# Performance work log

Hardware: AMD Instinct MI355X
Metric: run time of the kernel (lower is better)

## Reference

```python
import jax, jax.numpy as jnp
import numpy as np

MARGIN = 1.0
SAFE_RADIUS = 4.0
B, C, H, W = 16, 48, 64, 64
N_CORR = 2048


def _normalize(x, eps=1e-12):
    # F.normalize(x, dim=0): L2-normalize over the channel axis
    return x / jnp.maximum(jnp.linalg.norm(x, axis=0, keepdims=True), eps)


def _grid_positions(h, w):
    i, j = jnp.meshgrid(jnp.arange(h, dtype=jnp.float32),
                        jnp.arange(w, dtype=jnp.float32), indexing='ij')
    return jnp.stack([i.reshape(-1), j.reshape(-1)], axis=0)


def _per_image(df1, df2, att1, att2, ids, fp2):
    c, h1, w1 = df1.shape
    _, h2, w2 = df2.shape
    all_d1 = _normalize(df1.reshape(c, -1))   # [c, h1*w1]
    all_d2 = _normalize(df2.reshape(c, -1))   # [c, h2*w2]

    d1 = all_d1[:, ids]                       # [c, n] gathered anchors
    s1 = att1.reshape(-1)[ids]                # [n]
    d2 = _normalize(df2[:, fp2[0], fp2[1]])   # [c, n] gathered positives

    positive_distance = 2.0 - 2.0 * jnp.sum(d1 * d2, axis=0)  # [n]

    # hard-negative mining in image 2
    grid2 = _grid_positions(h2, w2)           # [2, h2*w2]
    pd2 = jnp.max(jnp.abs(fp2.astype(jnp.float32)[:, :, None] - grid2[:, None, :]), axis=0)
    out2 = (pd2 > SAFE_RADIUS).astype(df1.dtype)            # [n, h2*w2]
    dm2 = 2.0 - 2.0 * jnp.einsum('cn,cm->nm', d1, all_d2)   # [n, h2*w2]
    neg2 = jnp.min(dm2 + (1.0 - out2) * 10.0, axis=1)       # [n]

    # hard-negative mining in image 1
    grid1 = _grid_positions(h1, w1)
    fp1 = grid1[:, ids]                                      # [2, n]
    pd1 = jnp.max(jnp.abs(fp1[:, :, None] - grid1[:, None, :]), axis=0)
    out1 = (pd1 > SAFE_RADIUS).astype(df1.dtype)
    dm1 = 2.0 - 2.0 * jnp.einsum('cn,cm->nm', d2, all_d1)
    neg1 = jnp.min(dm1 + (1.0 - out1) * 10.0, axis=1)

    diff = positive_distance - jnp.minimum(neg1, neg2)
    s2 = att2[0, fp2[0], fp2[1]]
    w = s1 * s2
    return jnp.sum(w * jax.nn.relu(MARGIN + diff)) / jnp.sum(w)


def setup_inputs() -> dict:
    key = jax.random.key(0)
    k1, k2, k3, k4, k5, k6 = jax.random.split(key, 6)
    return {
        'x1_encoded': jax.random.normal(k1, (B, C, H, W), dtype=jnp.float32),
        'x2_encoded': jax.random.normal(k2, (B, C, H, W), dtype=jnp.float32),
        'attentions1': jax.random.uniform(k3, (B, 1, H, W), dtype=jnp.float32),
        'attentions2': jax.random.uniform(k4, (B, 1, H, W), dtype=jnp.float32),
        'ids': jax.random.randint(k5, (B, N_CORR), 0, H * W),
        'fmap_pos2': jax.random.randint(k6, (B, 2, N_CORR), 0, H),
    }


def reference(x1_encoded, x2_encoded, attentions1, attentions2, ids, fmap_pos2):
    per_image = jax.vmap(_per_image)(x1_encoded, x2_encoded, attentions1,
                                     attentions2, ids, fmap_pos2)
    return jnp.mean(per_image).reshape(1)
```

## Files before the change

### kernel.cpp

```cpp
#include <hip/hip_runtime.h>
#include <stdint.h>

#define BB 16
#define HW 4096
#define NC 2048
#define KB 96
#define GRPB 12288
#define IMGB 393216

typedef __attribute__((ext_vector_type(8))) __bf16 bf16x8;
typedef __attribute__((ext_vector_type(8))) short short8;
typedef __attribute__((ext_vector_type(4))) float floatx4;

static __device__ __forceinline__ unsigned short f2bf(float f) {
    unsigned u = __builtin_bit_cast(unsigned, f);
    unsigned r = u + 0x7fffu + ((u >> 16) & 1u);
    return (unsigned short)(r >> 16);
}

#define GLD16(g, l) __builtin_amdgcn_global_load_lds((const __attribute__((address_space(1))) void*)(g), (__attribute__((address_space(3))) void*)(l), 16, 0, 0)

__global__ void prep_fused(const float* __restrict__ x1, const float* __restrict__ x2,
                           const int* __restrict__ ids, const int* __restrict__ fp2,
                           unsigned short* __restrict__ dbp,
                           int* __restrict__ perm, int* __restrict__ qcol_s,
                           int* __restrict__ aqpack, unsigned int* __restrict__ maxs2enc,
                           unsigned int* __restrict__ done) {
    __shared__ __align__(16) unsigned char slab[24576 + 4096 + 1024];
    int bid = blockIdx.x, tid = threadIdx.x;
    if (bid < 512) {
        int img = bid >> 8;
        int b = (bid >> 4) & 15;
        int p0 = (bid & 15) * 256;
        int w = tid >> 6, l = tid & 63;
        const float* x = img ? x2 : x1;
        const float* base = x + ((size_t)b * 48 + w * 12) * HW + p0 + 4 * l;
        floatx4 v[12];
        floatx4 ps = {0.f, 0.f, 0.f, 0.f};
#pragma unroll
        for (int cc = 0; cc < 12; ++cc) {
            v[cc] = *(const floatx4*)(base + cc * HW);
#pragma unroll
            for (int q = 0; q < 4; ++q) ps[q] = fmaf(v[cc][q], v[cc][q], ps[q]);
        }
        float* psum = (float*)(slab + 24576);
        float* rbuf = (float*)(slab + 24576 + 4096);
        *(floatx4*)(psum + w * 256 + 4 * l) = ps;
        __syncthreads();
        float s = psum[tid] + psum[256 + tid] + psum[512 + tid] + psum[768 + tid];
        rbuf[tid] = 1.f / fmaxf(sqrtf(s), 1e-12f);
        __syncthreads();
        floatx4 rv = *(const floatx4*)(rbuf + 4 * l);
#pragma unroll
        for (int q = 0; q < 4; ++q) {
            unsigned u[6];
#pragma unroll
            for (int p = 0; p < 6; ++p) {
                u[p] = (unsigned)f2bf(v[2 * p][q] * rv[q]) |
                       ((unsigned)f2bf(v[2 * p + 1][q] * rv[q]) << 16);
            }
            unsigned char* dst = slab + (4 * l + q) * KB + w * 24;
            *(uint2*)(dst + 0)  = make_uint2(u[0], u[1]);
            *(uint2*)(dst + 8)  = make_uint2(u[2], u[3]);
            *(uint2*)(dst + 16) = make_uint2(u[4], u[5]);
        }
        __syncthreads();
        unsigned char* dstb = (unsigned char*)dbp + (size_t)(img * BB + b) * IMGB
                              + (p0 >> 7) * GRPB;
#pragma unroll
        for (int i = 0; i < 6; ++i) {
            int L = i * 4096 + tid * 16;
            int g = L / GRPB;
            int r = L - g * GRPB;
            int k = r >> 11;
            int c = (r & 2047) >> 4;
            *(floatx4*)(dstb + L) = *(const floatx4*)(slab + (g * 128 + c) * KB + k * 16);
        }
    } else if (bid < 544) {
        int* hist = (int*)slab;
        int* base = hist + 64;
        int seg = bid - 512;
        int dir = seg >> 4, b = seg & 15;
        if (tid < 64) hist[tid] = 0;
        __syncthreads();
#pragma unroll
        for (int k = 0; k < 8; ++k) {
            int n = k * 256 + tid;
            int idv = ids[b * NC + n];
            int i2 = fp2[b * 2 * NC + n];
            int qi = (dir == 0) ? i2 : (idv >> 6);
            atomicAdd(&hist[qi], 1);
        }
        __syncthreads();
        if (tid == 0) {
            int run = 0;
            for (int k = 0; k < 64; ++k) { base[k] = run; run += hist[k]; }
        }
        __syncthreads();
#pragma unroll
        for (int k = 0; k < 8; ++k) {
            int n = k * 256 + tid;
            int idv = ids[b * NC + n];
            int i2 = fp2[b * 2 * NC + n];
            int j2 = fp2[b * 2 * NC + NC + n];
            int qi, qj, qcol;
            if (dir == 0) { qi = i2; qj = j2; qcol = idv; }
            else          { qi = idv >> 6; qj = idv & 63; qcol = i2 * 64 + j2; }
            int slot = atomicAdd(&base[qi], 1);
            perm[seg * NC + slot] = n;
            qcol_s[seg * NC + slot] = qcol;
            aqpack[seg * NC + slot] = (qi << 8) | qj;
        }
    } else {
        int t = (bid - 544) * 256 + tid;
        uint4* p = (uint4*)maxs2enc;
        uint4 z = {0u, 0u, 0u, 0u};
#pragma unroll
        for (int k = 0; k < 8; ++k) p[k * 2048 + t] = z;
        if (t == 0) done[0] = 0u;
    }
}

#define TILEB 12288

static __device__ __forceinline__ void dma_tile(const unsigned char* g, unsigned char* l,
                                                int wave, int lane) {
#pragma unroll
    for (int rr = 0; rr < 3; ++rr)
        GLD16(g + rr * 4096 + wave * 1024 + lane * 16, l + rr * 4096 + wave * 1024);
}

__global__ __launch_bounds__(256, 4) void maxscore_mfma(
    const unsigned short* __restrict__ dbp,
    const int* __restrict__ perm, const int* __restrict__ qcol_s,
    const int* __restrict__ aqpack, unsigned int* __restrict__ maxs2enc) {
    __shared__ __align__(16) unsigned char smem[2 * TILEB];

    int tid = threadIdx.x, wave = tid >> 6, lane = tid & 63;
    int quad = lane >> 4, cl = lane & 15;
    int gid = blockIdx.x;
    int seg = gid & 31, dir = seg >> 4, b = seg & 15;
    int rest = gid >> 5, mtile = rest & 7, nq = rest >> 3;
    int qbase = mtile * 256;
    int dbimg = 1 - dir;

    const unsigned char* dbQ = (const unsigned char*)dbp + (size_t)(dir * BB + b) * IMGB;
    short8 z8 = {0, 0, 0, 0, 0, 0, 0, 0};
    short8 afr[4][2];
#pragma unroll
    for (int t = 0; t < 4; ++t) {
        int slot = qbase + wave * 64 + t * 16 + cl;
        int qc = qcol_s[seg * NC + slot];
        const unsigned char* src = dbQ + (qc >> 7) * GRPB + (qc & 127) * 16;
        afr[t][0] = *(const short8*)(src + quad * 2048);
        afr[t][1] = z8;
        if (quad < 2) afr[t][1] = *(const short8*)(src + (4 + quad) * 2048);
    }
    float qif[4][4], qjc[4][4];
    float cl_f = (float)cl;
#pragma unroll
    for (int t = 0; t < 4; ++t)
#pragma unroll
        for (int r = 0; r < 4; ++r) {
            int slot = qbase + wave * 64 + t * 16 + quad * 4 + r;
            int ap = aqpack[seg * NC + slot];
            qif[t][r] = (float)(ap >> 8);
            qjc[t][r] = (float)(ap & 255) - cl_f;
        }
    int wb = seg * NC + qbase + wave * 64;
    int qimin = __builtin_amdgcn_readfirstlane(aqpack[wb] >> 8);
    int qimax = __builtin_amdgcn_readfirstlane(aqpack[wb + 63] >> 8);

    const unsigned char* dbase = (const unsigned char*)dbp + (size_t)(dbimg * BB + b) * IMGB;
    dma_tile(dbase + (size_t)nq * GRPB, smem, wave, lane);

    const floatx4 zf = {0.f, 0.f, 0.f, 0.f};
    float mx[4][4];
#pragma unroll
    for (int t = 0; t < 4; ++t)
#pragma unroll
        for (int r = 0; r < 4; ++r) mx[t][r] = -1e30f;

    int b0_off = quad * 2048 + cl * 16;
    int b1_off = (4 + (quad & 1)) * 2048 + cl * 16;

    for (int tile = 0; tile < 8; ++tile) {
        unsigned char* buf = smem + (tile & 1) * TILEB;
        __syncthreads();
        if (tile + 1 < 8)
            dma_tile(dbase + (size_t)((tile + 1) * 4 + nq) * GRPB,
                     smem + ((tile + 1) & 1) * TILEB, wave, lane);
        int mi0 = (tile * 4 + nq) * 2;
#pragma unroll
        for (int half = 0; half < 2; ++half) {
            int mi = mi0 + half;
            bool active = (mi >= qimin - 4) && (mi <= qimax + 4);
            if (active) {
                float mi_f = (float)mi;
                bool rowok[4][4];
#pragma unroll
                for (int t = 0; t < 4; ++t)
#pragma unroll
                    for (int r = 0; r < 4; ++r)
                        rowok[t][r] = fabsf(qif[t][r] - mi_f) > 4.0f;
#pragma unroll
                for (int js = 0; js < 4; ++js) {
                    int sub = half * 4 + js;
                    float jj = (float)(js * 16);
                    short8 b0 = *(const short8*)(buf + b0_off + sub * 256);
                    short8 b1 = *(const short8*)(buf + b1_off + sub * 256);
#pragma unroll
                    for (int t = 0; t < 4; ++t) {
                        floatx4 acc = __builtin_amdgcn_mfma_f32_16x16x32_bf16(
                            __builtin_bit_cast(bf16x8, afr[t][0]),
                            __builtin_bit_cast(bf16x8, b0), zf, 0, 0, 0);
                        acc = __builtin_amdgcn_mfma_f32_16x16x32_bf16(
                            __builtin_bit_cast(bf16x8, afr[t][1]),
                            __builtin_bit_cast(bf16x8, b1), acc, 0, 0, 0);
#pragma unroll
                        for (int r = 0; r < 4; ++r) {
                            float dj = qjc[t][r] - jj;
                            bool ok = rowok[t][r] || (fabsf(dj) > 4.0f);
                            mx[t][r] = ok ? fmaxf(mx[t][r], acc[r]) : mx[t][r];
                        }
                    }
                }
            } else {
#pragma unroll
                for (int js = 0; js < 4; ++js) {
                    int sub = half * 4 + js;
                    short8 b0 = *(const short8*)(buf + b0_off + sub * 256);
                    short8 b1 = *(const short8*)(buf + b1_off + sub * 256);
#pragma unroll
                    for (int t = 0; t < 4; ++t) {
                        floatx4 acc = __builtin_amdgcn_mfma_f32_16x16x32_bf16(
                            __builtin_bit_cast(bf16x8, afr[t][0]),
                            __builtin_bit_cast(bf16x8, b0), zf, 0, 0, 0);
                        acc = __builtin_amdgcn_mfma_f32_16x16x32_bf16(
                            __builtin_bit_cast(bf16x8, afr[t][1]),
                            __builtin_bit_cast(bf16x8, b1), acc, 0, 0, 0);
#pragma unroll
                        for (int r = 0; r < 4; ++r)
                            mx[t][r] = fmaxf(mx[t][r], acc[r]);
                    }
                }
            }
        }
    }

#pragma unroll
    for (int t = 0; t < 4; ++t)
#pragma unroll
        for (int r = 0; r < 4; ++r) {
            float v = mx[t][r];
            v = fmaxf(v, __shfl_xor(v, 1, 16));
            v = fmaxf(v, __shfl_xor(v, 2, 16));
            v = fmaxf(v, __shfl_xor(v, 4, 16));
            v = fmaxf(v, __shfl_xor(v, 8, 16));
            mx[t][r] = v;
        }
    if (cl == 0) {
#pragma unroll
        for (int t = 0; t < 4; ++t)
#pragma unroll
            for (int r = 0; r < 4; ++r) {
                int slot = qbase + wave * 64 + t * 16 + quad * 4 + r;
                int orig = perm[seg * NC + slot];
                float v = mx[t][r] + 2.0f;
                atomicMax(&maxs2enc[(size_t)seg * NC + orig],
                          __builtin_bit_cast(unsigned, v));
            }
    }
}

__global__ void loss_kernel(const float* __restrict__ att1, const float* __restrict__ att2,
                            const int* __restrict__ ids, const int* __restrict__ fp2,
                            const unsigned short* __restrict__ dbp,
                            const unsigned int* __restrict__ maxs2enc,
                            float* __restrict__ pnum, float* __restrict__ pden,
                            unsigned int* __restrict__ done, float* __restrict__ out) {
    int b = blockIdx.x >> 3, chunk = blockIdx.x & 7;
    int tid = threadIdx.x;
    int n = chunk * 256 + tid;
    int idv = ids[b * NC + n];
    int i2 = fp2[b * 2 * NC + n], j2 = fp2[b * 2 * NC + NC + n];
    int c2 = i2 * 64 + j2;
    const unsigned char* a4 = (const unsigned char*)dbp + (size_t)(0 * BB + b) * IMGB
                              + (idv >> 7) * GRPB + (idv & 127) * 16;
    const unsigned char* b4 = (const unsigned char*)dbp + (size_t)(1 * BB + b) * IMGB
                              + (c2 >> 7) * GRPB + (c2 & 127) * 16;
    float dot = 0.f;
#pragma unroll
    for (int i = 0; i < 6; ++i) {
        uint4 xa = *(const uint4*)(a4 + i * 2048);
        uint4 xb = *(const uint4*)(b4 + i * 2048);
        const unsigned* xu = (const unsigned*)&xa;
        const unsigned* yu = (const unsigned*)&xb;
#pragma unroll
        for (int w = 0; w < 4; ++w) {
            float xl = __builtin_bit_cast(float, xu[w] << 16);
            float xh = __builtin_bit_cast(float, xu[w] & 0xffff0000u);
            float yl = __builtin_bit_cast(float, yu[w] << 16);
            float yh = __builtin_bit_cast(float, yu[w] & 0xffff0000u);
            dot = fmaf(xl, yl, fmaf(xh, yh, dot));
        }
    }
    float m0 = __builtin_bit_cast(float, maxs2enc[(size_t)(0 * BB + b) * NC + n]) - 2.0f;
    float m1 = __builtin_bit_cast(float, maxs2enc[(size_t)(1 * BB + b) * NC + n]) - 2.0f;
    float ms = fmaxf(m0, m1);
    float diff = (2.f - 2.f * dot) - (2.f - 2.f * ms);
    float w = att1[b * HW + idv] * att2[b * HW + c2];
    float num = w * fmaxf(0.f, 1.f + diff);
    float den = w;
    __shared__ float sn[256], sd[256];
    __shared__ int islast;
    sn[tid] = num; sd[tid] = den;
    __syncthreads();
    for (int s = 128; s > 0; s >>= 1) {
        if (tid < s) { sn[tid] += sn[tid + s]; sd[tid] += sd[tid + s]; }
        __syncthreads();
    }
    if (tid == 0) {
        pnum[blockIdx.x] = sn[0];
        pden[blockIdx.x] = sd[0];
        __threadfence();
        unsigned t = atomicAdd(done, 1u);
        islast = (t == 127u);
    }
    __syncthreads();
    if (islast) {
        __threadfence();
        if (tid < 16) {
            float nacc = 0.f, dacc = 0.f;
#pragma unroll
            for (int c = 0; c < 8; ++c) {
                nacc += pnum[tid * 8 + c];
                dacc += pden[tid * 8 + c];
            }
            sn[tid] = nacc / dacc;
        }
        __syncthreads();
        if (tid == 0) {
            float s = 0.f;
#pragma unroll
            for (int k = 0; k < 16; ++k) s += sn[k];
            out[0] = s * (1.f / BB);
        }
    }
}

extern "C" void kernel_launch(void* const* d_in, const int* in_sizes, int n_in,
                              void* d_out, int out_size, void* d_ws, size_t ws_size,
                              hipStream_t stream) {
    const float* x1  = (const float*)d_in[0];
    const float* x2  = (const float*)d_in[1];
    const float* att1 = (const float*)d_in[2];
    const float* att2 = (const float*)d_in[3];
    const int* ids   = (const int*)d_in[4];
    const int* fp2   = (const int*)d_in[5];
    float* out = (float*)d_out;

    unsigned char* w = (unsigned char*)d_ws;
    unsigned short* dbp = (unsigned short*)(w + 0);
    int* perm    = (int*)(w + 12582912);
    int* qcol_s  = (int*)(w + 12845056);
    int* aqpack  = (int*)(w + 13107200);
    unsigned int* maxs2enc = (unsigned int*)(w + 13369344);
    float* pnum  = (float*)(w + 13631488);
    float* pden  = (float*)(w + 13632000);
    unsigned int* done = (unsigned int*)(w + 13632512);

    prep_fused<<<dim3(552), dim3(256), 0, stream>>>(x1, x2, ids, fp2, dbp,
                                                    perm, qcol_s, aqpack, maxs2enc, done);
    maxscore_mfma<<<dim3(1024), dim3(256), 0, stream>>>(dbp, perm, qcol_s, aqpack, maxs2enc);
    loss_kernel<<<dim3(128), dim3(256), 0, stream>>>(att1, att2, ids, fp2, dbp, maxs2enc,
                                                     pnum, pden, done, out);
}
```

Measured before the change: 135.7 us.

## Switch hard-negative max-score GEMM to 32x32x16 MFMA tiles with packed query coords

Replaces the 16x16x32 bf16 MFMA tiling (4 row tiles × 2 K-steps, with the second K-step half zero-padded) with 32x32x16 MFMA (2 row tiles × 3 K-steps exactly covering 48 channels). This removes the wasted zero-padded K work and cuts B-fragment LDS reads per output. The exclusion mask now uses packed integer query coordinates with unsigned range compares instead of float abs tests. The epilogue reduction grows to 5 shuffles across 32 lanes, and more accumulator registers are live per wave, which may lower occupancy.

```diff
diff --git a/kernel.cpp b/kernel.cpp
--- a/kernel.cpp
+++ b/kernel.cpp
@@ -11,6 +11,7 @@
 typedef __attribute__((ext_vector_type(8))) __bf16 bf16x8;
 typedef __attribute__((ext_vector_type(8))) short short8;
 typedef __attribute__((ext_vector_type(4))) float floatx4;
+typedef __attribute__((ext_vector_type(16))) float floatx16;
 
 static __device__ __forceinline__ unsigned short f2bf(float f) {
     unsigned u = __builtin_bit_cast(unsigned, f);
@@ -137,52 +138,52 @@
     __shared__ __align__(16) unsigned char smem[2 * TILEB];
 
     int tid = threadIdx.x, wave = tid >> 6, lane = tid & 63;
-    int quad = lane >> 4, cl = lane & 15;
+    int hi = lane >> 5, lo = lane & 31;
     int gid = blockIdx.x;
     int seg = gid & 31, dir = seg >> 4, b = seg & 15;
     int rest = gid >> 5, mtile = rest & 7, nq = rest >> 3;
     int qbase = mtile * 256;
     int dbimg = 1 - dir;
+    int segb = seg * NC;
 
     const unsigned char* dbQ = (const unsigned char*)dbp + (size_t)(dir * BB + b) * IMGB;
-    short8 z8 = {0, 0, 0, 0, 0, 0, 0, 0};
-    short8 afr[4][2];
-#pragma unroll
-    for (int t = 0; t < 4; ++t) {
-        int slot = qbase + wave * 64 + t * 16 + cl;
-        int qc = qcol_s[seg * NC + slot];
+    short8 afr[2][3];
+#pragma unroll
+    for (int trow = 0; trow < 2; ++trow) {
+        int slot = qbase + wave * 64 + trow * 32 + lo;
+        int qc = qcol_s[segb + slot];
         const unsigned char* src = dbQ + (qc >> 7) * GRPB + (qc & 127) * 16;
-        afr[t][0] = *(const short8*)(src + quad * 2048);
-        afr[t][1] = z8;
-        if (quad < 2) afr[t][1] = *(const short8*)(src + (4 + quad) * 2048);
-    }
-    float qif[4][4], qjc[4][4];
-    float cl_f = (float)cl;
-#pragma unroll
-    for (int t = 0; t < 4; ++t)
-#pragma unroll
-        for (int r = 0; r < 4; ++r) {
-            int slot = qbase + wave * 64 + t * 16 + quad * 4 + r;
-            int ap = aqpack[seg * NC + slot];
-            qif[t][r] = (float)(ap >> 8);
-            qjc[t][r] = (float)(ap & 255) - cl_f;
-        }
-    int wb = seg * NC + qbase + wave * 64;
+#pragma unroll
+        for (int ks = 0; ks < 3; ++ks)
+            afr[trow][ks] = *(const short8*)(src + (2 * ks + hi) * 2048);
+    }
+    int app[2][8];
+#pragma unroll
+    for (int trow = 0; trow < 2; ++trow)
+#pragma unroll
+        for (int p = 0; p < 8; ++p) {
+            int r0 = 2 * p, r1 = r0 + 1;
+            int row0 = (r0 & 3) + 8 * (r0 >> 2) + 4 * hi;
+            int row1 = (r1 & 3) + 8 * (r1 >> 2) + 4 * hi;
+            int s0 = aqpack[segb + qbase + wave * 64 + trow * 32 + row0];
+            int s1 = aqpack[segb + qbase + wave * 64 + trow * 32 + row1];
+            app[trow][p] = (s0 & 0xffff) | (s1 << 16);
+        }
+    int wb = segb + qbase + wave * 64;
     int qimin = __builtin_amdgcn_readfirstlane(aqpack[wb] >> 8);
     int qimax = __builtin_amdgcn_readfirstlane(aqpack[wb + 63] >> 8);
 
     const unsigned char* dbase = (const unsigned char*)dbp + (size_t)(dbimg * BB + b) * IMGB;
     dma_tile(dbase + (size_t)nq * GRPB, smem, wave, lane);
 
-    const floatx4 zf = {0.f, 0.f, 0.f, 0.f};
-    float mx[4][4];
-#pragma unroll
-    for (int t = 0; t < 4; ++t)
-#pragma unroll
-        for (int r = 0; r < 4; ++r) mx[t][r] = -1e30f;
-
-    int b0_off = quad * 2048 + cl * 16;
-    int b1_off = (4 + (quad & 1)) * 2048 + cl * 16;
+    floatx16 zf16;
+#pragma unroll
+    for (int r = 0; r < 16; ++r) zf16[r] = 0.f;
+    float mx[2][16];
+#pragma unroll
+    for (int trow = 0; trow < 2; ++trow)
+#pragma unroll
+        for (int r = 0; r < 16; ++r) mx[trow][r] = -1e30f;
 
     for (int tile = 0; tile < 8; ++tile) {
         unsigned char* buf = smem + (tile & 1) * TILEB;
@@ -190,84 +191,80 @@
         if (tile + 1 < 8)
             dma_tile(dbase + (size_t)((tile + 1) * 4 + nq) * GRPB,
                      smem + ((tile + 1) & 1) * TILEB, wave, lane);
-        int mi0 = (tile * 4 + nq) * 2;
-#pragma unroll
-        for (int half = 0; half < 2; ++half) {
-            int mi = mi0 + half;
+        int g = tile * 4 + nq;
+#pragma unroll
+        for (int cb = 0; cb < 4; ++cb) {
+            int mi = 2 * g + (cb >> 1);
             bool active = (mi >= qimin - 4) && (mi <= qimax + 4);
+            short8 bfr[3];
+#pragma unroll
+            for (int ks = 0; ks < 3; ++ks)
+                bfr[ks] = *(const short8*)(buf + (2 * ks + hi) * 2048 + (cb * 32 + lo) * 16);
             if (active) {
-                float mi_f = (float)mi;
-                bool rowok[4][4];
-#pragma unroll
-                for (int t = 0; t < 4; ++t)
-#pragma unroll
-                    for (int r = 0; r < 4; ++r)
-                        rowok[t][r] = fabsf(qif[t][r] - mi_f) > 4.0f;
-#pragma unroll
-                for (int js = 0; js < 4; ++js) {
-                    int sub = half * 4 + js;
-                    float jj = (float)(js * 16);
-                    short8 b0 = *(const short8*)(buf + b0_off + sub * 256);
-                    short8 b1 = *(const short8*)(buf + b1_off + sub * 256);
-#pragma unroll
-                    for (int t = 0; t < 4; ++t) {
-                        floatx4 acc = __builtin_amdgcn_mfma_f32_16x16x32_bf16(
-                            __builtin_bit_cast(bf16x8, afr[t][0]),
-                            __builtin_bit_cast(bf16x8, b0), zf, 0, 0, 0);
-                        acc = __builtin_amdgcn_mfma_f32_16x16x32_bf16(
-                            __builtin_bit_cast(bf16x8, afr[t][1]),
-                            __builtin_bit_cast(bf16x8, b1), acc, 0, 0, 0);
-#pragma unroll
-                        for (int r = 0; r < 4; ++r) {
-                            float dj = qjc[t][r] - jj;
-                            bool ok = rowok[t][r] || (fabsf(dj) > 4.0f);
-                            mx[t][r] = ok ? fmaxf(mx[t][r], acc[r]) : mx[t][r];
-                        }
+                int jc = (cb & 1) * 32 + lo;
+#pragma unroll
+                for (int trow = 0; trow < 2; ++trow) {
+                    floatx16 acc = __builtin_amdgcn_mfma_f32_32x32x16_bf16(
+                        __builtin_bit_cast(bf16x8, afr[trow][0]),
+                        __builtin_bit_cast(bf16x8, bfr[0]), zf16, 0, 0, 0);
+                    acc = __builtin_amdgcn_mfma_f32_32x32x16_bf16(
+                        __builtin_bit_cast(bf16x8, afr[trow][1]),
+                        __builtin_bit_cast(bf16x8, bfr[1]), acc, 0, 0, 0);
+                    acc = __builtin_amdgcn_mfma_f32_32x32x16_bf16(
+                        __builtin_bit_cast(bf16x8, afr[trow][2]),
+                        __builtin_bit_cast(bf16x8, bfr[2]), acc, 0, 0, 0);
+#pragma unroll
+                    for (int r = 0; r < 16; ++r) {
+                        int pk = app[trow][r >> 1];
+                        int qi = (r & 1) ? ((pk >> 24) & 255) : ((pk >> 8) & 255);
+                        int qj = (r & 1) ? ((pk >> 16) & 255) : (pk & 255);
+                        bool ok = ((unsigned)(qi - mi + 4) > 8u) |
+                                  ((unsigned)(qj - jc + 4) > 8u);
+                        mx[trow][r] = ok ? fmaxf(mx[trow][r], acc[r]) : mx[trow][r];
                     }
                 }
             } else {
 #pragma unroll
-                for (int js = 0; js < 4; ++js) {
-                    int sub = half * 4 + js;
-                    short8 b0 = *(const short8*)(buf + b0_off + sub * 256);
-                    short8 b1 = *(const short8*)(buf + b1_off + sub * 256);
-#pragma unroll
-                    for (int t = 0; t < 4; ++t) {
-                        floatx4 acc = __builtin_amdgcn_mfma_f32_16x16x32_bf16(
-                            __builtin_bit_cast(bf16x8, afr[t][0]),
-                            __builtin_bit_cast(bf16x8, b0), zf, 0, 0, 0);
-                        acc = __builtin_amdgcn_mfma_f32_16x16x32_bf16(
-                            __builtin_bit_cast(bf16x8, afr[t][1]),
-                            __builtin_bit_cast(bf16x8, b1), acc, 0, 0, 0);
-#pragma unroll
-                        for (int r = 0; r < 4; ++r)
-                            mx[t][r] = fmaxf(mx[t][r], acc[r]);
-                    }
+                for (int trow = 0; trow < 2; ++trow) {
+                    floatx16 acc = __builtin_amdgcn_mfma_f32_32x32x16_bf16(
+                        __builtin_bit_cast(bf16x8, afr[trow][0]),
+                        __builtin_bit_cast(bf16x8, bfr[0]), zf16, 0, 0, 0);
+                    acc = __builtin_amdgcn_mfma_f32_32x32x16_bf16(
+                        __builtin_bit_cast(bf16x8, afr[trow][1]),
+                        __builtin_bit_cast(bf16x8, bfr[1]), acc, 0, 0, 0);
+                    acc = __builtin_amdgcn_mfma_f32_32x32x16_bf16(
+                        __builtin_bit_cast(bf16x8, afr[trow][2]),
+                        __builtin_bit_cast(bf16x8, bfr[2]), acc, 0, 0, 0);
+#pragma unroll
+                    for (int r = 0; r < 16; ++r)
+                        mx[trow][r] = fmaxf(mx[trow][r], acc[r]);
                 }
             }
         }
     }
 
 #pragma unroll
-    for (int t = 0; t < 4; ++t)
-#pragma unroll
-        for (int r = 0; r < 4; ++r) {
-            float v = mx[t][r];
-            v = fmaxf(v, __shfl_xor(v, 1, 16));
-            v = fmaxf(v, __shfl_xor(v, 2, 16));
-            v = fmaxf(v, __shfl_xor(v, 4, 16));
-            v = fmaxf(v, __shfl_xor(v, 8, 16));
-            mx[t][r] = v;
-        }
-    if (cl == 0) {
-#pragma unroll
-        for (int t = 0; t < 4; ++t)
-#pragma unroll
-            for (int r = 0; r < 4; ++r) {
-                int slot = qbase + wave * 64 + t * 16 + quad * 4 + r;
-                int orig = perm[seg * NC + slot];
-                float v = mx[t][r] + 2.0f;
-                atomicMax(&maxs2enc[(size_t)seg * NC + orig],
+    for (int trow = 0; trow < 2; ++trow)
+#pragma unroll
+        for (int r = 0; r < 16; ++r) {
+            float v = mx[trow][r];
+            v = fmaxf(v, __shfl_xor(v, 1, 32));
+            v = fmaxf(v, __shfl_xor(v, 2, 32));
+            v = fmaxf(v, __shfl_xor(v, 4, 32));
+            v = fmaxf(v, __shfl_xor(v, 8, 32));
+            v = fmaxf(v, __shfl_xor(v, 16, 32));
+            mx[trow][r] = v;
+        }
+    if (lo == 0) {
+#pragma unroll
+        for (int trow = 0; trow < 2; ++trow)
+#pragma unroll
+            for (int r = 0; r < 16; ++r) {
+                int row = (r & 3) + 8 * (r >> 2) + 4 * hi;
+                int slot = qbase + wave * 64 + trow * 32 + row;
+                int orig = perm[segb + slot];
+                float v = mx[trow][r] + 2.0f;
+                atomicMax(&maxs2enc[(size_t)segb + orig],
                           __builtin_bit_cast(unsigned, v));
             }
     }
```

New measurement: 409.2 us. +201.5%, slower.
